# Kernel tuning notes

Measured on AMD Instinct MI355X. Metric: run time of the kernel, lower is better.

## Reference

```python
import jax, jax.numpy as jnp
import numpy as np

B, T, C = 256, 1024, 64  # batch, n_steps, n_classes


def setup_inputs() -> dict:
    key = jax.random.key(0)
    k1, k2, k3, k4, k5 = jax.random.split(key, 5)
    x = jax.random.normal(k1, (B, T, C), dtype=jnp.float32)          # emission energies
    y = jax.random.randint(k2, (B, T), 0, C, dtype=jnp.int32)        # gold label path
    U = jax.random.normal(k3, (C, C), dtype=jnp.float32) * 0.1       # transition energies
    b_start = jax.random.normal(k4, (C,), dtype=jnp.float32) * 0.1   # start boundary energy
    b_end = jax.random.normal(k5, (C,), dtype=jnp.float32) * 0.1     # end boundary energy
    return {"x": x, "U": U, "b_start": b_start, "b_end": b_end, "y": y}


def reference(x, U, b_start, b_end, y):
    """sparse_chain_crf_loss (no mask): -(path_energy - free_energy), shape [B, 1]."""
    # add_boundary_energy: boost first/last timesteps
    x = x.at[:, 0, :].add(b_start)
    x = x.at[:, -1, :].add(b_end)

    # path_energy0: emission term + transition term along gold path
    emit = jnp.take_along_axis(x, y[:, :, None], axis=2)[..., 0].sum(axis=1)  # [B]
    trans = U[y[:, :-1], y[:, 1:]].sum(axis=1)                                # [B]
    path_energy = emit + trans

    # free_energy0: logsumexp forward recursion (linear-chain partition function)
    def step(alpha, xt):
        # alpha: [B, C] log-alpha at t-1; xt: [B, C] emissions at t
        alpha = jax.nn.logsumexp(alpha[:, :, None] + U[None, :, :] + xt[:, None, :], axis=1)
        return alpha, None

    xs = jnp.swapaxes(x[:, 1:, :], 0, 1)  # time-major [T-1, B, C]
    alpha_last, _ = jax.lax.scan(step, x[:, 0, :], xs)
    log_z = jax.nn.logsumexp(alpha_last, axis=-1)  # [B]

    return (-(path_energy - log_z))[:, None]  # [B, 1]
```

## Files before the change

### kernel.cpp

```cpp
#include <hip/hip_runtime.h>

namespace {

constexpr int kB = 256;
constexpr int kT = 1024;
constexpr int kC = 64;
constexpr int kSteps = 7;
constexpr int kRowStride = 136;
constexpr int kMaxRows = 259;

typedef _Float16 half1_t;
typedef _Float16 half4_t __attribute__((ext_vector_type(4)));
typedef float    f32x4  __attribute__((ext_vector_type(4)));

__device__ __forceinline__ float wave_sum(float v) {
#pragma unroll
  for (int off = 32; off >= 1; off >>= 1) v += __shfl_xor(v, off, 64);
  return v;
}
__device__ __forceinline__ float chain_max(float v) {
  v = fmaxf(v, __shfl_xor(v, 16, 64));
  v = fmaxf(v, __shfl_xor(v, 32, 64));
  return v;
}
__device__ __forceinline__ float chain_sum(float v) {
  v += __shfl_xor(v, 16, 64);
  v += __shfl_xor(v, 32, 64);
  return v;
}


__global__ __launch_bounds__(256) void crf_fused(
    const float* __restrict__ x,
    const float* __restrict__ U,
    const float* __restrict__ bs,
    const float* __restrict__ be,
    const int*   __restrict__ y,
    float*       __restrict__ wsf)
{
  const int bid = blockIdx.x;
  const int tid = threadIdx.x;
  const int wid = tid >> 6;
  const int j   = tid & 63;

  __shared__ __align__(16) char els[kMaxRows * kRowStride];

  const int b = bid >> 2;
  const int g = bid & 3;
  const int R1   = (g == 0) ? 1 : (256 * g - 2);
  const int rows = (g == 0) ? 256 : ((g == 3) ? 258 : 259);
  const int eoff = (g == 0) ? 3 : 0;
  const int elo  = eoff;
  const int ehi  = eoff + rows - 1;

  const float* xbase = x + (size_t)b * kT * kC;

  const int t0 = 256 * g + tid;
  const int* yrow = y + (size_t)b * kT;
  const int ym = (t0 > 0) ? yrow[t0 - 1] : 0;
  const int y0 = yrow[t0];

  {
    const float* xs = xbase + (size_t)R1 * kC;
    const int tail = rows * 16 - 4096;
    f32x4 vt;
    const bool hasTail = tid < tail;
    if (hasTail)
      vt = *reinterpret_cast<const f32x4*>(xs + (size_t)(4096 + tid) * 4);
    f32x4 v[16];
#pragma unroll
    for (int u = 0; u < 16; ++u)
      v[u] = *reinterpret_cast<const f32x4*>(xs + (size_t)(u * 256 + tid) * 4);
#pragma unroll
    for (int u = 0; u < 16; ++u) {
      const int idx = u * 256 + tid;
      half4_t hv;
      hv[0] = (half1_t)__expf(v[u][0]);
      hv[1] = (half1_t)__expf(v[u][1]);
      hv[2] = (half1_t)__expf(v[u][2]);
      hv[3] = (half1_t)__expf(v[u][3]);
      const int e  = (idx >> 4) + eoff;
      const int k0 = idx & 15;
      const int sw = ((e >> 4) & 7) << 4;
      *reinterpret_cast<half4_t*>(els + e * kRowStride + ((k0 * 8) ^ sw)) = hv;
    }
    if (hasTail) {
      const int idx = 4096 + tid;
      half4_t hv;
      hv[0] = (half1_t)__expf(vt[0]);
      hv[1] = (half1_t)__expf(vt[1]);
      hv[2] = (half1_t)__expf(vt[2]);
      hv[3] = (half1_t)__expf(vt[3]);
      const int e  = (idx >> 4) + eoff;
      const int k0 = idx & 15;
      const int sw = ((e >> 4) & 7) << 4;
      *reinterpret_cast<half4_t*>(els + e * kRowStride + ((k0 * 8) ^ sw)) = hv;
    }
  }

  const float peu = U[ym * kC + y0];

  const int q = j >> 4;
  const int r = j & 15;
  const int c = 64 * g + 16 * wid + r;

  half4_t W[4][4];
#pragma unroll
  for (int mb = 0; mb < 4; ++mb)
#pragma unroll
    for (int kb = 0; kb < 4; ++kb) {
      half4_t w;
#pragma unroll
      for (int i = 0; i < 4; ++i)
        w[i] = (half1_t)(0.25f * __expf(U[(16 * kb + 4 * q + i) * kC + 16 * mb + r]));
      W[mb][kb] = w;
    }

  float ebe[4][4];
#pragma unroll
  for (int mb = 0; mb < 4; ++mb)
#pragma unroll
    for (int i = 0; i < 4; ++i) ebe[mb][i] = __expf(be[16 * mb + 4 * q + i]);

  half4_t P[4];
#pragma unroll
  for (int kb = 0; kb < 4; ++kb) {
    half4_t p;
#pragma unroll
    for (int i = 0; i < 4; ++i) p[i] = (half1_t)1.0f;
    P[kb] = p;
  }
  int sacc = 0, eprev = 0;
  if (g == 0 && wid == 0) {
    float pv[4][4];
    float m0 = 0.f;
#pragma unroll
    for (int kb = 0; kb < 4; ++kb)
#pragma unroll
      for (int i = 0; i < 4; ++i) {
        const int cls = 16 * kb + 4 * q + i;
        const float vv = __expf(xbase[cls] + bs[cls]);
        pv[kb][i] = vv;
        m0 = fmaxf(m0, vv);
      }
    m0 = chain_max(m0);
    const int e0 = ((__float_as_uint(m0) >> 23) & 255) - 127;
    const float sc0 = __uint_as_float((unsigned)(127 - e0) << 23);
    if (r == 0) {
#pragma unroll
      for (int kb = 0; kb < 4; ++kb) {
        half4_t p;
#pragma unroll
        for (int i = 0; i < 4; ++i) p[i] = (half1_t)(pv[kb][i] * sc0);
        P[kb] = p;
      }
      sacc = e0;
    }
  }

  __syncthreads();

  float pe;
  {
    pe = 0.f;
    if (t0 >= 1) pe += peu;
    if (t0 == 0) {
      pe += xbase[y0] + bs[y0];
    } else {
      const int e = t0 - R1 + eoff;
      const int sw = ((e >> 4) & 7) << 4;
      const half1_t ev = *reinterpret_cast<const half1_t*>(
          els + e * kRowStride + ((((y0 >> 2) * 8) ^ sw) + (y0 & 3) * 2));
      pe += __logf((float)ev);
    }
    if (t0 == kT - 1) pe += be[y0];
    pe = wave_sum(pe);
    if (j == 0) wsf[(size_t)b * 272 + 256 + g * 4 + wid] = pe;
  }

  float ref = 0.f, fin = 0.f;
  const int ebase = 64 * wid + 4 * r;

#pragma unroll
  for (int s = 0; s < kSteps; ++s) {
    int e = ebase + s;
    e = (e < elo) ? elo : e;
    e = (e > ehi) ? ehi : e;
    const int sw = ((e >> 4) & 7) << 4;
    const char* rowp = els + e * kRowStride;
    uint2 Eh[4];
#pragma unroll
    for (int kb = 0; kb < 4; ++kb)
      Eh[kb] = *reinterpret_cast<const uint2*>(rowp + (((kb * 32) + q * 8) ^ sw));

    f32x4 D[4];
#pragma unroll
    for (int mb = 0; mb < 4; ++mb) {
      f32x4 d = {0.f, 0.f, 0.f, 0.f};
#pragma unroll
      for (int kb = 0; kb < 4; ++kb)
        d = __builtin_amdgcn_mfma_f32_16x16x16f16(W[mb][kb], P[kb], d, 0, 0, 0);
      D[mb] = d;
    }

    const float sc = __uint_as_float((unsigned)(127 - eprev) << 23);
    const bool active = !((c == 0 && s < 3) || (c == 255 && s == kSteps - 1));

    float m = 0.f;
    half4_t Pn[4];
#pragma unroll
    for (int mb = 0; mb < 4; ++mb) {
      const half4_t eh = __builtin_bit_cast(half4_t, Eh[mb]);
      half4_t p;
#pragma unroll
      for (int i = 0; i < 4; ++i) {
        float st = D[mb][i] * sc * (float)eh[i];
        if (s == 5) st *= (c == 255) ? ebe[mb][i] : 1.f;
        m = fmaxf(m, st);
        p[i] = (half1_t)st;
      }
      Pn[mb] = p;
    }
#pragma unroll
    for (int mb = 0; mb < 4; ++mb) P[mb] = active ? Pn[mb] : P[mb];
    sacc += active ? (eprev + 2) : 0;

    m = chain_max(m);
    const int en = ((__float_as_uint(m) >> 23) & 255) - 127;
    eprev = active ? en : eprev;

    if (s == 2 || s == kSteps - 1) {
      float Sv = 0.f;
#pragma unroll
      for (int mb = 0; mb < 4; ++mb)
#pragma unroll
        for (int i = 0; i < 4; ++i) Sv += (float)P[mb][i];
      Sv = chain_sum(Sv);
      const float lg = __log2f(Sv) + (float)sacc;
      if (s == 2) ref = (c == 0) ? 0.f : lg;
      else        fin = lg;
    }
  }

  if (q == 0) wsf[(size_t)b * 272 + c] = fin - ref;
}

__global__ __launch_bounds__(64, 1) void crf_combine(
    const float* __restrict__ wsf, float* __restrict__ out)
{
  const int b = blockIdx.x;
  const int j = threadIdx.x & 63;

  const float* row = wsf + (size_t)b * 272;
  float v = 0.69314718055994531f *
            (row[j] + row[j + 64] + row[j + 128] + row[j + 192]);
  if (j < 16) v -= row[256 + j];
  v = wave_sum(v);

  if (j == 0) out[b] = v;
}

}

extern "C" void kernel_launch(void* const* d_in, const int* in_sizes, int n_in,
                              void* d_out, int out_size, void* d_ws, size_t ws_size,
                              hipStream_t stream) {
  const float* x  = (const float*)d_in[0];
  const float* U  = (const float*)d_in[1];
  const float* bs = (const float*)d_in[2];
  const float* be = (const float*)d_in[3];
  const int*   y  = (const int*)d_in[4];
  float* out = (float*)d_out;
  float* wsf = (float*)d_ws;

  crf_fused<<<1024, 256, 0, stream>>>(x, U, bs, be, y, wsf);
  crf_combine<<<kB, 64, 0, stream>>>(wsf, out);
}
```

Measured before the change: 26.73 us.

## Stage raw fp32 emissions into LDS via direct global-to-LDS loads

Replaces the register-staged load, exp and fp16 pack of the emission tile with __builtin_amdgcn_global_load_lds, which copies raw fp32 rows straight into a 256-byte-stride, XOR-swizzled LDS buffer. The exp now runs lazily inside the step loop on the values each thread reads. The path-energy gather reads fp32 directly instead of taking the log of an fp16 exp. This removes register pressure and the store pass from the prologue, in exchange for doubling the LDS footprint and moving the exp work into the compute loop, where the overlapping windows mean some values are exponentiated more than once.

```diff
diff --git a/kernel.cpp b/kernel.cpp
--- a/kernel.cpp
+++ b/kernel.cpp
@@ -6,12 +6,14 @@
 constexpr int kT = 1024;
 constexpr int kC = 64;
 constexpr int kSteps = 7;
-constexpr int kRowStride = 136;
-constexpr int kMaxRows = 259;
+constexpr int kLdsRows = 272;
 
 typedef _Float16 half1_t;
 typedef _Float16 half4_t __attribute__((ext_vector_type(4)));
 typedef float    f32x4  __attribute__((ext_vector_type(4)));
+
+typedef const __attribute__((address_space(1))) void* gas_ptr;
+typedef __attribute__((address_space(3))) void* las_ptr;
 
 __device__ __forceinline__ float wave_sum(float v) {
 #pragma unroll
@@ -43,7 +45,7 @@
   const int wid = tid >> 6;
   const int j   = tid & 63;
 
-  __shared__ __align__(16) char els[kMaxRows * kRowStride];
+  __shared__ __align__(16) char els[kLdsRows * 256];
 
   const int b = bid >> 2;
   const int g = bid & 3;
@@ -62,39 +64,19 @@
 
   {
     const float* xs = xbase + (size_t)R1 * kC;
-    const int tail = rows * 16 - 4096;
-    f32x4 vt;
-    const bool hasTail = tid < tail;
-    if (hasTail)
-      vt = *reinterpret_cast<const f32x4*>(xs + (size_t)(4096 + tid) * 4);
-    f32x4 v[16];
-#pragma unroll
-    for (int u = 0; u < 16; ++u)
-      v[u] = *reinterpret_cast<const f32x4*>(xs + (size_t)(u * 256 + tid) * 4);
-#pragma unroll
-    for (int u = 0; u < 16; ++u) {
-      const int idx = u * 256 + tid;
-      half4_t hv;
-      hv[0] = (half1_t)__expf(v[u][0]);
-      hv[1] = (half1_t)__expf(v[u][1]);
-      hv[2] = (half1_t)__expf(v[u][2]);
-      hv[3] = (half1_t)__expf(v[u][3]);
-      const int e  = (idx >> 4) + eoff;
-      const int k0 = idx & 15;
-      const int sw = ((e >> 4) & 7) << 4;
-      *reinterpret_cast<half4_t*>(els + e * kRowStride + ((k0 * 8) ^ sw)) = hv;
-    }
-    if (hasTail) {
-      const int idx = 4096 + tid;
-      half4_t hv;
-      hv[0] = (half1_t)__expf(vt[0]);
-      hv[1] = (half1_t)__expf(vt[1]);
-      hv[2] = (half1_t)__expf(vt[2]);
-      hv[3] = (half1_t)__expf(vt[3]);
-      const int e  = (idx >> 4) + eoff;
-      const int k0 = idx & 15;
-      const int sw = ((e >> 4) & 7) << 4;
-      *reinterpret_cast<half4_t*>(els + e * kRowStride + ((k0 * 8) ^ sw)) = hv;
+#pragma unroll
+    for (int i = 0; i < 17; ++i) {
+      const int ql = (i * 4 + wid) * 64 + j;
+      int e = ql >> 4;
+      e = (e > ehi) ? ehi : e;
+      int n = e - eoff;
+      n = (n < 0) ? 0 : n;
+      const int ksrc = (ql & 15) ^ ((e >> 2) & 7);
+      const float* gp = xs + (size_t)n * kC + ksrc * 4;
+      __builtin_amdgcn_global_load_lds(
+          (gas_ptr)gp,
+          (las_ptr)(els + (size_t)(i * 4 + wid) * 1024),
+          16, 0, 0);
     }
   }
 
@@ -168,10 +150,8 @@
       pe += xbase[y0] + bs[y0];
     } else {
       const int e = t0 - R1 + eoff;
-      const int sw = ((e >> 4) & 7) << 4;
-      const half1_t ev = *reinterpret_cast<const half1_t*>(
-          els + e * kRowStride + ((((y0 >> 2) * 8) ^ sw) + (y0 & 3) * 2));
-      pe += __logf((float)ev);
+      const int ky = (y0 >> 2) ^ ((e >> 2) & 7);
+      pe += *reinterpret_cast<const float*>(els + e * 256 + ky * 16 + (y0 & 3) * 4);
     }
     if (t0 == kT - 1) pe += be[y0];
     pe = wave_sum(pe);
@@ -186,12 +166,12 @@
     int e = ebase + s;
     e = (e < elo) ? elo : e;
     e = (e > ehi) ? ehi : e;
-    const int sw = ((e >> 4) & 7) << 4;
-    const char* rowp = els + e * kRowStride;
-    uint2 Eh[4];
-#pragma unroll
-    for (int kb = 0; kb < 4; ++kb)
-      Eh[kb] = *reinterpret_cast<const uint2*>(rowp + (((kb * 32) + q * 8) ^ sw));
+    const int sw3 = (e >> 2) & 7;
+    const char* rowp = els + e * 256;
+    f32x4 Ex[4];
+#pragma unroll
+    for (int mb = 0; mb < 4; ++mb)
+      Ex[mb] = *reinterpret_cast<const f32x4*>(rowp + (((4 * mb + q) ^ sw3) * 16));
 
     f32x4 D[4];
 #pragma unroll
@@ -210,11 +190,10 @@
     half4_t Pn[4];
 #pragma unroll
     for (int mb = 0; mb < 4; ++mb) {
-      const half4_t eh = __builtin_bit_cast(half4_t, Eh[mb]);
       half4_t p;
 #pragma unroll
       for (int i = 0; i < 4; ++i) {
-        float st = D[mb][i] * sc * (float)eh[i];
+        float st = D[mb][i] * sc * __expf(Ex[mb][i]);
         if (s == 5) st *= (c == 255) ? ebe[mb][i] : 1.f;
         m = fmaxf(m, st);
         p[i] = (half1_t)st;
```

Result: slower. 29.49 us (+10.3%).
